# Performance work log

Measured on AMD Instinct MI355X. Metric: run time of the kernel, lower is better.

Reference implementation:

```python
import jax, jax.numpy as jnp
import numpy as np

TLEN, BSZ, HID = 64, 32, 1024
SLEN = 200
V_TGT = 32000
V_EXT = 2000
UNK = 0  # ext_dict UNK index, ignored in the onehot scatter


def setup_inputs() -> dict:
    key = jax.random.key(0)
    ks = jax.random.split(key, 6)
    hidden = jax.random.normal(ks[0], (TLEN, BSZ, HID), dtype=jnp.float32)
    attn = jax.random.uniform(ks[1], (TLEN, BSZ, SLEN), dtype=jnp.float32)
    attn = attn / jnp.sum(attn, axis=-1, keepdims=True)  # attention-like distribution
    copy_to_ext = jax.random.randint(ks[2], (SLEN, BSZ), 0, V_EXT)
    W_out = jax.random.normal(ks[3], (V_TGT, HID), dtype=jnp.float32) * 0.02
    b_out = jnp.zeros((V_TGT,), dtype=jnp.float32)
    w_copy = jax.random.normal(ks[4], (1, HID), dtype=jnp.float32) * 0.02
    b_copy = jnp.zeros((1,), dtype=jnp.float32)
    return {"hidden": hidden, "attn": attn, "copy_to_ext": copy_to_ext,
            "W_out": W_out, "b_out": b_out, "w_copy": w_copy, "b_copy": b_copy}


def _safe_log(v):
    return jnp.log(jnp.clip(v, 0.001, 1.0 - 0.001))


def reference(hidden, attn, copy_to_ext, W_out, b_out, w_copy, b_copy):
    tlen, bsz, hid = hidden.shape
    slen = attn.shape[-1]
    h = hidden.reshape(tlen * bsz, hid)
    a = attn.reshape(tlen * bsz, slen)

    # p(copy) gate
    copy = jax.nn.sigmoid(h @ w_copy.T + b_copy)            # [N, 1]
    # generator log-probs over tgt vocab
    logits = h @ W_out.T + b_out                            # [N, V_TGT]
    prob_log = jax.nn.log_softmax(logits, axis=-1)
    out_prob_log = prob_log + _safe_log(copy)

    # attention mass scaled by (1 - p(copy)) -- NOTE: matches source exactly
    mul_attn = a * (1.0 - copy)                             # [N, SLEN]
    mul_attn_b = mul_attn.reshape(tlen, bsz, slen).transpose(1, 0, 2)  # [B, T, S]
    idx = copy_to_ext.T                                     # [B, S]

    def per_batch(m, i):
        # m: [T, S], i: [S]; scatter-add attn mass into ext vocab, ignoring UNK
        valid = (i != UNK).astype(m.dtype)                  # onehot ignore_index
        return jax.ops.segment_sum((m * valid).T, i, num_segments=V_EXT).T  # [T, E]

    ext_copy_prob = jax.vmap(per_batch)(mul_attn_b, idx)    # [B, T, E]
    ext_copy_prob = ext_copy_prob.transpose(1, 0, 2).reshape(tlen * bsz, V_EXT)
    ext_copy_prob_log = _safe_log(ext_copy_prob)

    out = jnp.concatenate([out_prob_log, ext_copy_prob_log], axis=1)
    return out.reshape(tlen, bsz, V_TGT + V_EXT)
```

## Files before the change

### kernel.cpp

```cpp
#include <hip/hip_runtime.h>
#include <cstdint>
#include <cstddef>

#define TLEN 64
#define BSZ  32
#define NROW 2048
#define HID  1024
#define SLEN 200
#define VT   32000
#define VE   2000
#define OUTW 34000
#define NBN  250

typedef float  f32x4  __attribute__((ext_vector_type(4)));
typedef __bf16 bf16x4 __attribute__((ext_vector_type(4)));
typedef __bf16 bf16x8 __attribute__((ext_vector_type(8)));
typedef float  floatx4 __attribute__((ext_vector_type(4)));

__global__ __launch_bounds__(256) void prep_kernel(
    const float* __restrict__ h, const float* __restrict__ wc,
    const float* __restrict__ bc, const float* __restrict__ W,
    __bf16* __restrict__ Hbf, __bf16* __restrict__ Wbf,
    float* __restrict__ logcopy, float* __restrict__ oneminus) {
  int tid = threadIdx.x;
  if (blockIdx.x < NROW) {
    int row = blockIdx.x;
    f32x4 v  = ((const f32x4*)(h + (size_t)row * HID))[tid];
    f32x4 wv = ((const f32x4*)wc)[tid];
    bf16x4 o;
    o.x = (__bf16)v.x; o.y = (__bf16)v.y; o.z = (__bf16)v.z; o.w = (__bf16)v.w;
    ((bf16x4*)(Hbf + (size_t)row * HID))[tid] = o;
    float s = v.x * wv.x + v.y * wv.y + v.z * wv.z + v.w * wv.w;
    #pragma unroll
    for (int off = 32; off; off >>= 1) s += __shfl_down(s, off, 64);
    __shared__ float wsum[4];
    int lane = tid & 63, w = tid >> 6;
    if (lane == 0) wsum[w] = s;
    __syncthreads();
    if (tid == 0) {
      float x = wsum[0] + wsum[1] + wsum[2] + wsum[3] + bc[0];
      float pc = 1.f / (1.f + __expf(-x));
      float pcc = fminf(fmaxf(pc, 0.001f), 0.999f);
      logcopy[row]  = logf(pcc);
      oneminus[row] = 1.f - pc;
    }
  } else {
    const int n4 = (VT * HID) / 4;
    int i = (blockIdx.x - NROW) * 256 + tid;
    for (; i < n4; i += 4096 * 256) {
      f32x4 v = __builtin_nontemporal_load(((const f32x4*)W) + i);
      bf16x4 o;
      o.x = (__bf16)v.x; o.y = (__bf16)v.y; o.z = (__bf16)v.z; o.w = (__bf16)v.w;
      ((bf16x4*)Wbf)[i] = o;
    }
  }
}

#define BM 128
#define BN 128
#define BK 32

__device__ __forceinline__ void load_lds16(const __bf16* g, __bf16* s) {
  __builtin_amdgcn_global_load_lds(
      (const __attribute__((address_space(1))) void*)g,
      (__attribute__((address_space(3))) void*)s, 16, 0, 0);
}

__global__ __launch_bounds__(256) void gemm_kernel(
    const __bf16* __restrict__ A, const __bf16* __restrict__ B,
    const float* __restrict__ bias, float* __restrict__ out) {
  __shared__ __attribute__((aligned(16))) __bf16 As[BM * BK];
  __shared__ __attribute__((aligned(16))) __bf16 Bs[BN * BK];
  __shared__ float lS0[128], lS1[128];

  const int tid = threadIdx.x;
  const int bn = blockIdx.x;
  const int bm = blockIdx.y;
  const int K = HID;

  const __bf16* aptr0 = A + (size_t)(bm * BM + (tid >> 2)) * K + (tid & 3) * 8;
  const __bf16* aptr1 = aptr0 + (size_t)64 * K;
  const __bf16* bptr0 = B + (size_t)(bn * BN + (tid >> 2)) * K + (tid & 3) * 8;
  const __bf16* bptr1 = bptr0 + (size_t)64 * K;
  __bf16* alds0 = &As[tid * 8];
  __bf16* alds1 = &As[2048 + tid * 8];
  __bf16* blds0 = &Bs[tid * 8];
  __bf16* blds1 = &Bs[2048 + tid * 8];

  const int l  = tid & 63;
  const int w  = tid >> 6;
  const int wm = w & 1;
  const int wn = w >> 1;
  const int lr = l & 15;
  const int q  = l >> 4;

  const bf16x8* Asv = (const bf16x8*)As;
  const bf16x8* Bsv = (const bf16x8*)Bs;

  int aidx[4], bidx[4];
  #pragma unroll
  for (int i = 0; i < 4; i++) aidx[i] = (wm * 64 + i * 16 + lr) * 4 + q;
  #pragma unroll
  for (int j = 0; j < 4; j++) bidx[j] = (wn * 64 + j * 16 + lr) * 4 + q;

  floatx4 acc[4][4] = {};

  for (int kt = 0; kt < K; kt += BK) {
    load_lds16(aptr0 + kt, alds0);
    load_lds16(aptr1 + kt, alds1);
    load_lds16(bptr0 + kt, blds0);
    load_lds16(bptr1 + kt, blds1);
    __syncthreads();

    bf16x8 af[4], bfr[4];
    #pragma unroll
    for (int i = 0; i < 4; i++) af[i] = Asv[aidx[i]];
    #pragma unroll
    for (int j = 0; j < 4; j++) bfr[j] = Bsv[bidx[j]];

    #pragma unroll
    for (int i = 0; i < 4; i++)
      #pragma unroll
      for (int j = 0; j < 4; j++)
        acc[i][j] = __builtin_amdgcn_mfma_f32_16x16x32_bf16(af[i], bfr[j], acc[i][j], 0, 0, 0);

    __syncthreads();
  }

  const int col0 = bn * BN + wn * 64 + lr;
  const int row0 = bm * BM + wm * 64 + q * 4;
  float bv[4];
  #pragma unroll
  for (int j = 0; j < 4; j++) bv[j] = bias[col0 + j * 16];

  #pragma unroll
  for (int i = 0; i < 4; i++) {
    #pragma unroll
    for (int r = 0; r < 4; r++) {
      int m = row0 + i * 16 + r;
      float* po = out + (size_t)m * OUTW + col0;
      float vj[4];
      #pragma unroll
      for (int j = 0; j < 4; j++) vj[j] = acc[i][j][r] + bv[j];
      #pragma unroll
      for (int j = 0; j < 4; j++) __builtin_nontemporal_store(vj[j], po + j * 16);
      float s4 = __expf(vj[0]) + __expf(vj[1]) + __expf(vj[2]) + __expf(vj[3]);
      #pragma unroll
      for (int off = 1; off < 16; off <<= 1) s4 += __shfl_xor(s4, off, 64);
      if (lr == 0) {
        int rl = wm * 64 + i * 16 + q * 4 + r;
        if (wn == 0) lS0[rl] = s4; else lS1[rl] = s4;
      }
    }
  }
  __syncthreads();
  if (w == 0) {
    #pragma unroll
    for (int e0 = 0; e0 < 128; e0 += 64) {
      int e = e0 + l;
      float S = lS0[e] + lS1[e];
      int m = bm * BM + e;
      __builtin_nontemporal_store(S, out + (size_t)m * OUTW + VT + bn);
    }
  }
}

__global__ __launch_bounds__(256) void finish_kernel(
    const float* __restrict__ attn, const int* __restrict__ c2e,
    const float* __restrict__ logcopy, const float* __restrict__ oneminus,
    float* __restrict__ out) {
  __shared__ float ext[VE];
  __shared__ float rS[4];
  int row = blockIdx.x;
  int tid = threadIdx.x;
  int b = row & (BSZ - 1);
  float* orow = out + (size_t)row * OUTW;

  for (int e = tid; e < VE; e += 256) ext[e] = 0.f;

  float S = (tid < NBN) ? orow[VT + tid] : 0.f;
  #pragma unroll
  for (int off = 32; off; off >>= 1) S += __shfl_down(S, off, 64);
  int lane = tid & 63, w = tid >> 6;
  if (lane == 0) rS[w] = S;
  __syncthreads();
  float sub = logf(rS[0] + rS[1] + rS[2] + rS[3]) - logcopy[row];

  float om1 = oneminus[row];
  if (tid < SLEN) {
    int idx = c2e[tid * BSZ + b];
    if (idx != 0)
      atomicAdd(&ext[idx], attn[(size_t)row * SLEN + tid] * om1);
  }

  #pragma unroll 4
  for (int k2 = 0; k2 < 31; k2++) {
    f32x4* p = (f32x4*)orow + (tid + k2 * 256);
    f32x4 v = __builtin_nontemporal_load(p);
    v = v - sub;
    __builtin_nontemporal_store(v, p);
  }
  {
    float v = __builtin_nontemporal_load(orow + 31744 + tid);
    __builtin_nontemporal_store(v - sub, orow + 31744 + tid);
  }

  __syncthreads();
  for (int e = tid; e < VE; e += 256)
    __builtin_nontemporal_store(logf(fminf(fmaxf(ext[e], 0.001f), 0.999f)),
                                orow + VT + e);
}

extern "C" void kernel_launch(void* const* d_in, const int* in_sizes, int n_in,
                              void* d_out, int out_size, void* d_ws, size_t ws_size,
                              hipStream_t stream) {
  const float* hidden = (const float*)d_in[0];
  const float* attn   = (const float*)d_in[1];
  const int*   c2e    = (const int*)d_in[2];
  const float* W      = (const float*)d_in[3];
  const float* bout   = (const float*)d_in[4];
  const float* wc     = (const float*)d_in[5];
  const float* bc     = (const float*)d_in[6];
  float* out = (float*)d_out;

  char* ws = (char*)d_ws;
  __bf16* Hbf = (__bf16*)ws;
  __bf16* Wbf = (__bf16*)(ws + 4194304);
  float* logcopy  = (float*)(ws + 4194304 + 65536000);
  float* oneminus = logcopy + NROW;

  prep_kernel<<<NROW + 4096, 256, 0, stream>>>(hidden, wc, bc, W, Hbf, Wbf,
                                               logcopy, oneminus);
  gemm_kernel<<<dim3(VT / BN, NROW / BM), 256, 0, stream>>>(Hbf, Wbf, bout, out);
  finish_kernel<<<NROW, 256, 0, stream>>>(attn, c2e, logcopy, oneminus, out);
}
```

Measured before the change: 685.8 us.

## Double-buffer GEMM LDS tiles, swizzle block order, use cached stores for logits

```diff
diff --git a/kernel.cpp b/kernel.cpp
--- a/kernel.cpp
+++ b/kernel.cpp
@@ -69,23 +69,20 @@
 __global__ __launch_bounds__(256) void gemm_kernel(
     const __bf16* __restrict__ A, const __bf16* __restrict__ B,
     const float* __restrict__ bias, float* __restrict__ out) {
-  __shared__ __attribute__((aligned(16))) __bf16 As[BM * BK];
-  __shared__ __attribute__((aligned(16))) __bf16 Bs[BN * BK];
+  __shared__ __attribute__((aligned(16))) __bf16 As[2][BM * BK];
+  __shared__ __attribute__((aligned(16))) __bf16 Bs[2][BN * BK];
   __shared__ float lS0[128], lS1[128];
 
   const int tid = threadIdx.x;
-  const int bn = blockIdx.x;
-  const int bm = blockIdx.y;
+  const int swz = (blockIdx.x & 7) * 500 + (blockIdx.x >> 3);
+  const int bm = swz & 15;
+  const int bn = swz >> 4;
   const int K = HID;
 
   const __bf16* aptr0 = A + (size_t)(bm * BM + (tid >> 2)) * K + (tid & 3) * 8;
   const __bf16* aptr1 = aptr0 + (size_t)64 * K;
   const __bf16* bptr0 = B + (size_t)(bn * BN + (tid >> 2)) * K + (tid & 3) * 8;
   const __bf16* bptr1 = bptr0 + (size_t)64 * K;
-  __bf16* alds0 = &As[tid * 8];
-  __bf16* alds1 = &As[2048 + tid * 8];
-  __bf16* blds0 = &Bs[tid * 8];
-  __bf16* blds1 = &Bs[2048 + tid * 8];
 
   const int l  = tid & 63;
   const int w  = tid >> 6;
@@ -94,9 +91,6 @@
   const int lr = l & 15;
   const int q  = l >> 4;
 
-  const bf16x8* Asv = (const bf16x8*)As;
-  const bf16x8* Bsv = (const bf16x8*)Bs;
-
   int aidx[4], bidx[4];
   #pragma unroll
   for (int i = 0; i < 4; i++) aidx[i] = (wm * 64 + i * 16 + lr) * 4 + q;
@@ -105,19 +99,26 @@
 
   floatx4 acc[4][4] = {};
 
-  for (int kt = 0; kt < K; kt += BK) {
-    load_lds16(aptr0 + kt, alds0);
-    load_lds16(aptr1 + kt, alds1);
-    load_lds16(bptr0 + kt, blds0);
-    load_lds16(bptr1 + kt, blds1);
-    __syncthreads();
-
+  load_lds16(aptr0, &As[0][tid * 8]);
+  load_lds16(aptr1, &As[0][2048 + tid * 8]);
+  load_lds16(bptr0, &Bs[0][tid * 8]);
+  load_lds16(bptr1, &Bs[0][2048 + tid * 8]);
+  __syncthreads();
+
+  int p = 0;
+  for (int kt = BK; kt < K; kt += BK) {
+    load_lds16(aptr0 + kt, &As[p ^ 1][tid * 8]);
+    load_lds16(aptr1 + kt, &As[p ^ 1][2048 + tid * 8]);
+    load_lds16(bptr0 + kt, &Bs[p ^ 1][tid * 8]);
+    load_lds16(bptr1 + kt, &Bs[p ^ 1][2048 + tid * 8]);
+
+    const bf16x8* Asv = (const bf16x8*)As[p];
+    const bf16x8* Bsv = (const bf16x8*)Bs[p];
     bf16x8 af[4], bfr[4];
     #pragma unroll
     for (int i = 0; i < 4; i++) af[i] = Asv[aidx[i]];
     #pragma unroll
     for (int j = 0; j < 4; j++) bfr[j] = Bsv[bidx[j]];
-
     #pragma unroll
     for (int i = 0; i < 4; i++)
       #pragma unroll
@@ -125,6 +126,22 @@
         acc[i][j] = __builtin_amdgcn_mfma_f32_16x16x32_bf16(af[i], bfr[j], acc[i][j], 0, 0, 0);
 
     __syncthreads();
+    p ^= 1;
+  }
+
+  {
+    const bf16x8* Asv = (const bf16x8*)As[p];
+    const bf16x8* Bsv = (const bf16x8*)Bs[p];
+    bf16x8 af[4], bfr[4];
+    #pragma unroll
+    for (int i = 0; i < 4; i++) af[i] = Asv[aidx[i]];
+    #pragma unroll
+    for (int j = 0; j < 4; j++) bfr[j] = Bsv[bidx[j]];
+    #pragma unroll
+    for (int i = 0; i < 4; i++)
+      #pragma unroll
+      for (int j = 0; j < 4; j++)
+        acc[i][j] = __builtin_amdgcn_mfma_f32_16x16x32_bf16(af[i], bfr[j], acc[i][j], 0, 0, 0);
   }
 
   const int col0 = bn * BN + wn * 64 + lr;
@@ -143,7 +160,7 @@
       #pragma unroll
       for (int j = 0; j < 4; j++) vj[j] = acc[i][j][r] + bv[j];
       #pragma unroll
-      for (int j = 0; j < 4; j++) __builtin_nontemporal_store(vj[j], po + j * 16);
+      for (int j = 0; j < 4; j++) po[j * 16] = vj[j];
       float s4 = __expf(vj[0]) + __expf(vj[1]) + __expf(vj[2]) + __expf(vj[3]);
       #pragma unroll
       for (int off = 1; off < 16; off <<= 1) s4 += __shfl_xor(s4, off, 64);
@@ -160,7 +177,7 @@
       int e = e0 + l;
       float S = lS0[e] + lS1[e];
       int m = bm * BM + e;
-      __builtin_nontemporal_store(S, out + (size_t)m * OUTW + VT + bn);
+      out[(size_t)m * OUTW + VT + bn] = S;
     }
   }
 }
@@ -176,9 +193,10 @@
   int b = row & (BSZ - 1);
   float* orow = out + (size_t)row * OUTW;
 
+  float S = (tid < NBN) ? orow[VT + tid] : 0.f;
+
   for (int e = tid; e < VE; e += 256) ext[e] = 0.f;
 
-  float S = (tid < NBN) ? orow[VT + tid] : 0.f;
   #pragma unroll
   for (int off = 32; off; off >>= 1) S += __shfl_down(S, off, 64);
   int lane = tid & 63, w = tid >> 6;
@@ -196,12 +214,12 @@
   #pragma unroll 4
   for (int k2 = 0; k2 < 31; k2++) {
     f32x4* p = (f32x4*)orow + (tid + k2 * 256);
-    f32x4 v = __builtin_nontemporal_load(p);
+    f32x4 v = *p;
     v = v - sub;
     __builtin_nontemporal_store(v, p);
   }
   {
-    float v = __builtin_nontemporal_load(orow + 31744 + tid);
+    float v = orow[31744 + tid];
     __builtin_nontemporal_store(v - sub, orow + 31744 + tid);
   }
 
@@ -231,6 +249,6 @@
 
   prep_kernel<<<NROW + 4096, 256, 0, stream>>>(hidden, wc, bc, W, Hbf, Wbf,
                                                logcopy, oneminus);
-  gemm_kernel<<<dim3(VT / BN, NROW / BM), 256, 0, stream>>>(Hbf, Wbf, bout, out);
+  gemm_kernel<<<VT / BN * (NROW / BM), 256, 0, stream>>>(Hbf, Wbf, bout, out);
   finish_kernel<<<NROW, 256, 0, stream>>>(attn, c2e, logcopy, oneminus, out);
 }
```

Result: faster. 632.6 us (-7.8%).

## Rewrite GEMM with 256x256 tiles, double-buffered LDS, XOR swizzle and block swizzle

Applied to the files above, without the earlier changes.

```diff
diff --git a/kernel.cpp b/kernel.cpp
--- a/kernel.cpp
+++ b/kernel.cpp
@@ -10,7 +10,13 @@
 #define VT   32000
 #define VE   2000
 #define OUTW 34000
-#define NBN  250
+
+#define BM 256
+#define BN 256
+#define BK 64
+#define NMT 8
+#define NNT 125
+#define NBN 125
 
 typedef float  f32x4  __attribute__((ext_vector_type(4)));
 typedef __bf16 bf16x4 __attribute__((ext_vector_type(4)));
@@ -56,9 +62,6 @@
   }
 }
 
-#define BM 128
-#define BN 128
-#define BK 32
 
 __device__ __forceinline__ void load_lds16(const __bf16* g, __bf16* s) {
   __builtin_amdgcn_global_load_lds(
@@ -66,103 +69,157 @@
       (__attribute__((address_space(3))) void*)s, 16, 0, 0);
 }
 
-__global__ __launch_bounds__(256) void gemm_kernel(
+__device__ __forceinline__ void loadB4(const __bf16* Sb, int offB, int ga,
+                                       bf16x8 bfr[4]) {
+  #pragma unroll
+  for (int j = 0; j < 4; j++)
+    bfr[j] = *(const bf16x8*)(Sb + offB + j * 1024 + ga);
+}
+
+template<int RG>
+__device__ __forceinline__ void loadA4(const __bf16* Sa, int offA, int ga,
+                                       bf16x8 af[4]) {
+  #pragma unroll
+  for (int i = 0; i < 4; i++)
+    af[i] = *(const bf16x8*)(Sa + offA + (RG * 4 + i) * 1024 + ga);
+}
+
+template<int RG>
+__device__ __forceinline__ void mfma16(floatx4 (&acc)[8][4], const bf16x8 af[4],
+                                       const bf16x8 bfr[4]) {
+  __builtin_amdgcn_s_setprio(1);
+  #pragma unroll
+  for (int i = 0; i < 4; i++)
+    #pragma unroll
+    for (int j = 0; j < 4; j++)
+      acc[RG * 4 + i][j] =
+          __builtin_amdgcn_mfma_f32_16x16x32_bf16(af[i], bfr[j],
+                                                  acc[RG * 4 + i][j], 0, 0, 0);
+  __builtin_amdgcn_s_setprio(0);
+}
+
+#define VM2 asm volatile("s_waitcnt vmcnt(2)" ::: "memory")
+#define VM0 asm volatile("s_waitcnt vmcnt(0)" ::: "memory")
+
+__global__ __launch_bounds__(512) void gemm_kernel(
     const __bf16* __restrict__ A, const __bf16* __restrict__ B,
     const float* __restrict__ bias, float* __restrict__ out) {
-  __shared__ __attribute__((aligned(16))) __bf16 As[BM * BK];
-  __shared__ __attribute__((aligned(16))) __bf16 Bs[BN * BK];
-  __shared__ float lS0[128], lS1[128];
+  __shared__ __attribute__((aligned(16))) __bf16 Asb[2][BM * BK];
+  __shared__ __attribute__((aligned(16))) __bf16 Bsb[2][BN * BK];
 
   const int tid = threadIdx.x;
-  const int bn = blockIdx.x;
-  const int bm = blockIdx.y;
-  const int K = HID;
-
-  const __bf16* aptr0 = A + (size_t)(bm * BM + (tid >> 2)) * K + (tid & 3) * 8;
-  const __bf16* aptr1 = aptr0 + (size_t)64 * K;
-  const __bf16* bptr0 = B + (size_t)(bn * BN + (tid >> 2)) * K + (tid & 3) * 8;
-  const __bf16* bptr1 = bptr0 + (size_t)64 * K;
-  __bf16* alds0 = &As[tid * 8];
-  __bf16* alds1 = &As[2048 + tid * 8];
-  __bf16* blds0 = &Bs[tid * 8];
-  __bf16* blds1 = &Bs[2048 + tid * 8];
-
-  const int l  = tid & 63;
-  const int w  = tid >> 6;
+  const int swz = ((int)blockIdx.x & 7) * 125 + ((int)blockIdx.x >> 3);
+  const int bm = swz & 7;
+  const int bn = swz >> 3;
+
+  const int r0s = tid >> 3,         g0 = tid & 7;
+  const int r1s = (512 + tid) >> 3, g1 = (512 + tid) & 7;
+  const int gs0 = (g0 ^ (r0s & 7)) * 8;
+  const int gs1 = (g1 ^ (r1s & 7)) * 8;
+
+  const __bf16* Abase = A + (size_t)bm * BM * HID;
+  const __bf16* Bbase = B + (size_t)bn * BN * HID;
+
+  const int l = tid & 63, w = tid >> 6;
   const int wm = w & 1;
   const int wn = w >> 1;
-  const int lr = l & 15;
-  const int q  = l >> 4;
-
-  const bf16x8* Asv = (const bf16x8*)As;
-  const bf16x8* Bsv = (const bf16x8*)Bs;
-
-  int aidx[4], bidx[4];
-  #pragma unroll
-  for (int i = 0; i < 4; i++) aidx[i] = (wm * 64 + i * 16 + lr) * 4 + q;
-  #pragma unroll
-  for (int j = 0; j < 4; j++) bidx[j] = (wn * 64 + j * 16 + lr) * 4 + q;
-
-  floatx4 acc[4][4] = {};
-
-  for (int kt = 0; kt < K; kt += BK) {
-    load_lds16(aptr0 + kt, alds0);
-    load_lds16(aptr1 + kt, alds1);
-    load_lds16(bptr0 + kt, blds0);
-    load_lds16(bptr1 + kt, blds1);
-    __syncthreads();
-
-    bf16x8 af[4], bfr[4];
-    #pragma unroll
-    for (int i = 0; i < 4; i++) af[i] = Asv[aidx[i]];
-    #pragma unroll
-    for (int j = 0; j < 4; j++) bfr[j] = Bsv[bidx[j]];
-
-    #pragma unroll
-    for (int i = 0; i < 4; i++)
-      #pragma unroll
-      for (int j = 0; j < 4; j++)
-        acc[i][j] = __builtin_amdgcn_mfma_f32_16x16x32_bf16(af[i], bfr[j], acc[i][j], 0, 0, 0);
-
-    __syncthreads();
-  }
+  const int lr = l & 15, q = l >> 4;
+  const int x7 = lr & 7;
+  const int offA = (wm * 128 + lr) * 64;
+  const int offB = (wn * 64 + lr) * 64;
+  const int ga0 = (q ^ x7) * 8;
+  const int ga1 = ((4 + q) ^ x7) * 8;
+
+#define STAGE_A(dst, h, kt) do { \
+    load_lds16(Abase + (size_t)((h) * 128 + r0s) * HID + (kt) * 64 + gs0, \
+               (dst) + (h) * 8192 + tid * 8); \
+    load_lds16(Abase + (size_t)((h) * 128 + r1s) * HID + (kt) * 64 + gs1, \
+               (dst) + (h) * 8192 + 4096 + tid * 8); \
+  } while (0)
+#define STAGE_B(dst, h, kt) do { \
+    load_lds16(Bbase + (size_t)((h) * 128 + r0s) * HID + (kt) * 64 + gs0, \
+               (dst) + (h) * 8192 + tid * 8); \
+    load_lds16(Bbase + (size_t)((h) * 128 + r1s) * HID + (kt) * 64 + gs1, \
+               (dst) + (h) * 8192 + 4096 + tid * 8); \
+  } while (0)
+
+  bf16x8 af[4], bfr[4];
+  floatx4 acc[8][4] = {};
+
+#define TILE_BLOCK(CA, CB, SA, SB, stk, DOST, VMASM) do {                    \
+                                                       \
+    if (DOST) STAGE_A(SA, 0, stk);                                           \
+    VMASM;                                                                   \
+    __builtin_amdgcn_s_barrier();                                            \
+    loadB4(CB, offB, ga0, bfr);                                              \
+    loadA4<0>(CA, offA, ga0, af);                                            \
+    mfma16<0>(acc, af, bfr);                                                 \
+    __builtin_amdgcn_s_barrier();                                            \
+                                                       \
+    loadA4<1>(CA, offA, ga0, af);                                            \
+    if (DOST) STAGE_A(SA, 1, stk);                                           \
+    __builtin_amdgcn_s_barrier();                                            \
+    mfma16<1>(acc, af, bfr);                                                 \
+    __builtin_amdgcn_s_barrier();                                            \
+                                                       \
+    loadB4(CB, offB, ga1, bfr);                                              \
+    loadA4<0>(CA, offA, ga1, af);                                            \
+    if (DOST) STAGE_B(SB, 0, stk);                                           \
+    __builtin_amdgcn_s_barrier();                                            \
+    mfma16<0>(acc, af, bfr);                                                 \
+    __builtin_amdgcn_s_barrier();                                            \
+                                                       \
+    loadA4<1>(CA, offA, ga1, af);                                            \
+    if (DOST) STAGE_B(SB, 1, stk);                                           \
+    __builtin_amdgcn_s_barrier();                                            \
+    mfma16<1>(acc, af, bfr);                                                 \
+    __builtin_amdgcn_s_barrier();                                            \
+  } while (0)
+
+  STAGE_A(Asb[0], 0, 0); STAGE_A(Asb[0], 1, 0);
+  STAGE_B(Bsb[0], 0, 0); STAGE_B(Bsb[0], 1, 0);
+
+  for (int i = 0; i < 7; i++) {
+    TILE_BLOCK(Asb[0], Bsb[0], Asb[1], Bsb[1], 2 * i + 1, true, VM2);
+    TILE_BLOCK(Asb[1], Bsb[1], Asb[0], Bsb[0], 2 * i + 2, true, VM2);
+  }
+  TILE_BLOCK(Asb[0], Bsb[0], Asb[1], Bsb[1], 15, true, VM2);
+  TILE_BLOCK(Asb[1], Bsb[1], Asb[0], Bsb[0], 0, false, VM0);
+
+  __syncthreads();
+  float* lS = (float*)Asb;
 
   const int col0 = bn * BN + wn * 64 + lr;
-  const int row0 = bm * BM + wm * 64 + q * 4;
+  const int row0 = bm * BM + wm * 128 + q * 4;
   float bv[4];
   #pragma unroll
   for (int j = 0; j < 4; j++) bv[j] = bias[col0 + j * 16];
 
   #pragma unroll
-  for (int i = 0; i < 4; i++) {
+  for (int fi = 0; fi < 8; fi++) {
     #pragma unroll
     for (int r = 0; r < 4; r++) {
-      int m = row0 + i * 16 + r;
+      int m = row0 + fi * 16 + r;
       float* po = out + (size_t)m * OUTW + col0;
       float vj[4];
       #pragma unroll
-      for (int j = 0; j < 4; j++) vj[j] = acc[i][j][r] + bv[j];
+      for (int j = 0; j < 4; j++) vj[j] = acc[fi][j][r] + bv[j];
       #pragma unroll
-      for (int j = 0; j < 4; j++) __builtin_nontemporal_store(vj[j], po + j * 16);
+      for (int j = 0; j < 4; j++) po[j * 16] = vj[j];
       float s4 = __expf(vj[0]) + __expf(vj[1]) + __expf(vj[2]) + __expf(vj[3]);
       #pragma unroll
       for (int off = 1; off < 16; off <<= 1) s4 += __shfl_xor(s4, off, 64);
-      if (lr == 0) {
-        int rl = wm * 64 + i * 16 + q * 4 + r;
-        if (wn == 0) lS0[rl] = s4; else lS1[rl] = s4;
-      }
+      if (lr == 0) lS[wn * BM + wm * 128 + fi * 16 + q * 4 + r] = s4;
     }
   }
   __syncthreads();
-  if (w == 0) {
-    #pragma unroll
-    for (int e0 = 0; e0 < 128; e0 += 64) {
-      int e = e0 + l;
-      float S = lS0[e] + lS1[e];
-      int m = bm * BM + e;
-      __builtin_nontemporal_store(S, out + (size_t)m * OUTW + VT + bn);
-    }
-  }
+  if (tid < BM) {
+    float S = lS[tid] + lS[BM + tid] + lS[2 * BM + tid] + lS[3 * BM + tid];
+    out[(size_t)(bm * BM + tid) * OUTW + VT + bn] = S;
+  }
+#undef TILE_BLOCK
+#undef STAGE_A
+#undef STAGE_B
 }
 
 __global__ __launch_bounds__(256) void finish_kernel(
@@ -176,9 +233,10 @@
   int b = row & (BSZ - 1);
   float* orow = out + (size_t)row * OUTW;
 
+  float S = (tid < NBN) ? orow[VT + tid] : 0.f;
+
   for (int e = tid; e < VE; e += 256) ext[e] = 0.f;
 
-  float S = (tid < NBN) ? orow[VT + tid] : 0.f;
   #pragma unroll
   for (int off = 32; off; off >>= 1) S += __shfl_down(S, off, 64);
   int lane = tid & 63, w = tid >> 6;
@@ -196,12 +254,12 @@
   #pragma unroll 4
   for (int k2 = 0; k2 < 31; k2++) {
     f32x4* p = (f32x4*)orow + (tid + k2 * 256);
-    f32x4 v = __builtin_nontemporal_load(p);
+    f32x4 v = *p;
     v = v - sub;
     __builtin_nontemporal_store(v, p);
   }
   {
-    float v = __builtin_nontemporal_load(orow + 31744 + tid);
+    float v = orow[31744 + tid];
     __builtin_nontemporal_store(v - sub, orow + 31744 + tid);
   }
 
@@ -231,6 +289,6 @@
 
   prep_kernel<<<NROW + 4096, 256, 0, stream>>>(hidden, wc, bc, W, Hbf, Wbf,
                                                logcopy, oneminus);
-  gemm_kernel<<<dim3(VT / BN, NROW / BM), 256, 0, stream>>>(Hbf, Wbf, bout, out);
+  gemm_kernel<<<NMT * NNT, 512, 0, stream>>>(Hbf, Wbf, bout, out);
   finish_kernel<<<NROW, 256, 0, stream>>>(attn, c2e, logcopy, oneminus, out);
 }
```

Measured after the change: 590.1 us. 1.16x faster.
